# Performance work log

Hardware: AMD Instinct MI355X
Metric: run time of the kernel (lower is better)

Reference implementation:

```python
import jax, jax.numpy as jnp
import numpy as np

RADIUS = 400.0
FIELD = 8000.0  # um extent of slide coordinate field


def setup_inputs() -> dict:
    key = jax.random.key(0)
    ks = jax.random.split(key, 8)
    B, N, D, H, K = 4, 4096, 1536, 512, 8
    images = jax.random.normal(ks[0], (B, N, D), dtype=jnp.float32)
    positions = jax.random.uniform(ks[1], (B, N, 2), dtype=jnp.float32) * FIELD
    W_feat = jax.random.normal(ks[2], (D, H), dtype=jnp.float32) * (1.0 / np.sqrt(D))
    b_feat = jnp.zeros((H,), dtype=jnp.float32)
    W_pos = jax.random.normal(ks[3], (2, H), dtype=jnp.float32) * 0.5
    W_gnn = jax.random.normal(ks[4], (H, H), dtype=jnp.float32) * (1.0 / np.sqrt(H))
    W_self = jax.random.normal(ks[5], (H, H), dtype=jnp.float32) * (1.0 / np.sqrt(H))
    anchors = jax.random.normal(ks[6], (K, D), dtype=jnp.float32)
    return {"images": images, "positions": positions, "W_feat": W_feat,
            "b_feat": b_feat, "W_pos": W_pos, "W_gnn": W_gnn,
            "W_self": W_self, "anchors": anchors}


def _radius_adjacency(pos):
    # pos: (N, 2). Dense O(N^2) radius graph (mirrors torch.cdist + mask).
    sq = jnp.sum(pos * pos, axis=-1)                       # (N,)
    d2 = sq[:, None] + sq[None, :] - 2.0 * (pos @ pos.T)   # (N, N)
    mask = d2 < (RADIUS * RADIUS)
    N = pos.shape[0]
    mask = mask & ~jnp.eye(N, dtype=bool)                  # no self-loops
    return mask.astype(pos.dtype)


def reference(images, positions, W_feat, b_feat, W_pos, W_gnn, W_self, anchors):
    # --- Stream A: explicit concept quantifier (cosine sim to anchors) ---
    x_norm = images / jnp.clip(jnp.linalg.norm(images, axis=-1, keepdims=True), 1e-12)
    a_norm = anchors / jnp.clip(jnp.linalg.norm(anchors, axis=-1, keepdims=True), 1e-12)
    scores = jnp.einsum('bnd,kd->bnk', x_norm, a_norm)     # (B, N, K)
    concept_profile = scores.mean(axis=1)                  # (B, K)

    # --- Stream B: feature extraction with positional encoding ---
    feat = images @ W_feat + b_feat + positions @ W_pos    # (B, N, H)

    # --- radius graph + one mean-aggregation GNN layer, per slide ---
    def per_graph(f, p):
        A = _radius_adjacency(p)                           # (N, N)
        deg = jnp.clip(A.sum(axis=-1, keepdims=True), 1.0) # (N, 1)
        h = jax.nn.relu(f)
        agg = (A @ h) / deg                                # mean over neighbors
        return jax.nn.relu(agg @ W_gnn + f @ W_self)       # (N, H)

    refined = jax.vmap(per_graph)(feat, positions)         # (B, N, H)
    latent_spatial = refined.mean(axis=1)                  # (B, H)  per-graph mean pool

    return jnp.concatenate([latent_spatial, concept_profile], axis=1)  # (B, H+K)
```

## Files before the change

### kernel.cpp

```cpp
#include <hip/hip_runtime.h>

#define B_ 4
#define N_ 4096
#define D_ 1536
#define H_ 512
#define K_ 8
#define M_ (B_*N_)
#define R2_ 160000.0f

typedef __attribute__((ext_vector_type(8))) short bf16x8;
typedef __attribute__((ext_vector_type(4))) float f32x4;

__device__ __forceinline__ unsigned short f2bf(float f) {
  union { float f; unsigned u; } v; v.f = f;
  unsigned r = (v.u + 0x7FFFu + ((v.u >> 16) & 1u)) >> 16;
  return (unsigned short)r;
}
__device__ __forceinline__ float bf2f(unsigned short s) {
  union { unsigned u; float f; } v; v.u = ((unsigned)s) << 16; return v.f;
}

typedef const __attribute__((address_space(1))) unsigned int gas_u32;
typedef __attribute__((address_space(3))) unsigned int las_u32;
__device__ __forceinline__ void gl_lds16(const unsigned short* g, unsigned short* l) {
  __builtin_amdgcn_global_load_lds((gas_u32*)g, (las_u32*)l, 16, 0, 0);
}

__global__ void k_anorm(const float* __restrict__ anchors, float* __restrict__ anorm) {
  int k = blockIdx.x; int lane = threadIdx.x;
  float s = 0.f;
  for (int i = lane; i < D_; i += 64) { float v = anchors[k*D_ + i]; s += v*v; }
  #pragma unroll
  for (int off = 32; off; off >>= 1) s += __shfl_down(s, off);
  if (lane == 0) anorm[k] = fmaxf(sqrtf(s), 1e-12f);
}

__global__ void k_transpose(const float* __restrict__ W, unsigned short* __restrict__ WT,
                            int Krows, int outStride, int outOff) {
  __shared__ float t[64][65];
  int bx = blockIdx.x;
  int by = blockIdx.y;
  int tid = threadIdx.x;
  int tx = tid & 63, ty = tid >> 6;
  #pragma unroll
  for (int r = 0; r < 64; r += 4)
    t[ty + r][tx] = W[(size_t)(by*64 + ty + r)*H_ + bx*64 + tx];
  __syncthreads();
  #pragma unroll
  for (int r = 0; r < 64; r += 4) {
    int n = bx*64 + ty + r;
    WT[(size_t)n*outStride + outOff + by*64 + tx] = f2bf(t[tx][ty + r]);
  }
}

__global__ __launch_bounds__(256) void k_concept_cast(
    const float* __restrict__ images, const float* __restrict__ anchors,
    const float* __restrict__ anorm, unsigned short* __restrict__ imgs_bf,
    float* __restrict__ out) {
  __shared__ float sA[K_*D_];
  __shared__ float sc[4][K_];
  int tid = threadIdx.x, lane = tid & 63, w = tid >> 6;
  {
    const float4* a4 = (const float4*)anchors;
    float4* sA4 = (float4*)sA;
    #pragma unroll
    for (int i = 0; i < 12; i++) sA4[tid + 256*i] = a4[tid + 256*i];
  }
  __syncthreads();
  float acc_k[K_] = {};
  for (int r = 0; r < 8; r++) {
    int gm = blockIdx.x*32 + w*8 + r;
    const float4* xrow = (const float4*)(images + (size_t)gm*D_);
    float nrm = 0.f; float dot[K_] = {};
    #pragma unroll
    for (int it = 0; it < 6; it++) {
      int j = lane + 64*it;
      float4 x = xrow[j];
      nrm += x.x*x.x + x.y*x.y + x.z*x.z + x.w*x.w;
      #pragma unroll
      for (int k = 0; k < K_; k++) {
        float4 a = *(const float4*)&sA[(size_t)(k*384 + j)*4];
        dot[k] += x.x*a.x + x.y*a.y + x.z*a.z + x.w*a.w;
      }
      ushort4 s;
      s.x = f2bf(x.x); s.y = f2bf(x.y); s.z = f2bf(x.z); s.w = f2bf(x.w);
      *(ushort4*)&imgs_bf[(size_t)gm*D_ + (size_t)j*4] = s;
    }
    #pragma unroll
    for (int off = 32; off; off >>= 1) {
      nrm += __shfl_down(nrm, off);
      #pragma unroll
      for (int k = 0; k < K_; k++) dot[k] += __shfl_down(dot[k], off);
    }
    if (lane == 0) {
      float inv = 1.0f / fmaxf(sqrtf(nrm), 1e-12f);
      #pragma unroll
      for (int k = 0; k < K_; k++) acc_k[k] += dot[k] * inv / anorm[k];
    }
  }
  if (lane == 0) {
    #pragma unroll
    for (int k = 0; k < K_; k++) sc[w][k] = acc_k[k];
  }
  __syncthreads();
  if (tid < K_) {
    float s = sc[0][tid] + sc[1][tid] + sc[2][tid] + sc[3][tid];
    int b = blockIdx.x >> 7;
    atomicAdd(out + b*(H_+K_) + H_ + tid, s * (1.0f/N_));
  }
}

#define BM 128
#define BN 128
#define BK 32

__global__ __launch_bounds__(256) void k_gemm(
    const unsigned short* __restrict__ A, const unsigned short* __restrict__ BT,
    int Kdim, int mode, const float* __restrict__ bias, const float* __restrict__ Wpos,
    const float* __restrict__ positions, unsigned short* __restrict__ AB,
    float* __restrict__ out) {
  __shared__ unsigned short As[BM*BK];
  __shared__ unsigned short Bs[BN*BK];
  __shared__ float colsum[BN];
  int tid = threadIdx.x;
  int lane = tid & 63, wv = tid >> 6;
  int wm = wv >> 1, wn = wv & 1;
  int l15 = lane & 15, quad = lane >> 4;
  int bx = blockIdx.x;
  int bm = bx & 127, bn = bx >> 7;
  int m0 = bm*BM, n0 = bn*BN;

  f32x4 acc[4][4] = {};

  int c = wv*2;
  int rowc = (lane >> 2), seg = lane & 3;
  const unsigned short* gA0 = A  + (size_t)(m0 + c*16 + rowc)*Kdim + seg*8;
  const unsigned short* gA1 = gA0 + (size_t)16*Kdim;
  const unsigned short* gB0 = BT + (size_t)(n0 + c*16 + rowc)*Kdim + seg*8;
  const unsigned short* gB1 = gB0 + (size_t)16*Kdim;
  unsigned short* lA0 = As + c*512;
  unsigned short* lA1 = lA0 + 512;
  unsigned short* lB0 = Bs + c*512;
  unsigned short* lB1 = lB0 + 512;

  int nk = Kdim / BK;
  for (int kt = 0; kt < nk; kt++) {
    __syncthreads();
    gl_lds16(gA0, lA0); gl_lds16(gA1, lA1);
    gl_lds16(gB0, lB0); gl_lds16(gB1, lB1);
    gA0 += BK; gA1 += BK; gB0 += BK; gB1 += BK;
    __syncthreads();

    bf16x8 aF[4], bF[4];
    #pragma unroll
    for (int f = 0; f < 4; f++)
      aF[f] = *(const bf16x8*)&As[(wm*64 + f*16 + l15)*BK + quad*8];
    #pragma unroll
    for (int f = 0; f < 4; f++)
      bF[f] = *(const bf16x8*)&Bs[(wn*64 + f*16 + l15)*BK + quad*8];
    #pragma unroll
    for (int mi = 0; mi < 4; mi++)
      #pragma unroll
      for (int ni = 0; ni < 4; ni++)
        acc[mi][ni] = __builtin_amdgcn_mfma_f32_16x16x32_bf16(aF[mi], bF[ni], acc[mi][ni], 0, 0, 0);
  }

  if (mode == 0) {
    #pragma unroll
    for (int ni = 0; ni < 4; ni++) {
      int gh = n0 + wn*64 + ni*16 + l15;
      float bz = bias[gh];
      float w0 = Wpos[gh];
      float w1 = Wpos[H_ + gh];
      #pragma unroll
      for (int mi = 0; mi < 4; mi++) {
        #pragma unroll
        for (int r = 0; r < 4; r++) {
          int gm = m0 + wm*64 + mi*16 + quad*4 + r;
          float px = positions[(size_t)gm*2];
          float py = positions[(size_t)gm*2 + 1];
          float v = acc[mi][ni][r] + bz + px*w0 + py*w1;
          AB[(size_t)gm*1024 + 512 + gh] = f2bf(v);
        }
      }
    }
  } else {
    if (tid < BN) colsum[tid] = 0.f;
    __syncthreads();
    #pragma unroll
    for (int ni = 0; ni < 4; ni++) {
      float s = 0.f;
      #pragma unroll
      for (int mi = 0; mi < 4; mi++) {
        #pragma unroll
        for (int r = 0; r < 4; r++) s += fmaxf(acc[mi][ni][r], 0.f);
      }
      s += __shfl_down(s, 32);
      s += __shfl_down(s, 16);
      if (quad == 0) atomicAdd(&colsum[wn*64 + ni*16 + l15], s);
    }
    __syncthreads();
    if (tid < BN) {
      int b = m0 >> 12;
      atomicAdd(out + b*(H_+K_) + n0 + tid, colsum[tid] * (1.0f/N_));
    }
  }
}

__global__ void k_aggregate(const float* __restrict__ positions,
                            unsigned short* __restrict__ AB) {
  __shared__ unsigned short nlist[N_];
  __shared__ int cnt;
  int gm = blockIdx.x;
  int b = gm >> 12, i = gm & 4095;
  int tid = threadIdx.x;
  if (tid == 0) cnt = 0;
  __syncthreads();
  const float* pos = positions + (size_t)b*N_*2;
  float xi = pos[(size_t)i*2], yi = pos[(size_t)i*2 + 1];
  for (int j = tid; j < N_; j += 256) {
    float dx = pos[(size_t)j*2] - xi;
    float dy = pos[(size_t)j*2 + 1] - yi;
    float d2 = dx*dx + dy*dy;
    if (d2 < R2_ && j != i) {
      int p = atomicAdd(&cnt, 1);
      nlist[p] = (unsigned short)j;
    }
  }
  __syncthreads();
  int deg = cnt;
  float inv = 1.0f / (float)(deg > 1 ? deg : 1);
  float a0 = 0.f, a1 = 0.f;
  const unsigned short* featbase = AB + (size_t)(b << 12)*1024 + 512 + tid*2;
  for (int n = 0; n < deg; n++) {
    int j = nlist[n];
    unsigned v = *(const unsigned*)(featbase + (size_t)j*1024);
    a0 += fmaxf(bf2f((unsigned short)(v & 0xFFFFu)), 0.f);
    a1 += fmaxf(bf2f((unsigned short)(v >> 16)), 0.f);
  }
  unsigned o0 = f2bf(a0*inv), o1 = f2bf(a1*inv);
  *(unsigned*)(AB + (size_t)gm*1024 + tid*2) = (o1 << 16) | o0;
}

extern "C" void kernel_launch(void* const* d_in, const int* in_sizes, int n_in,
                              void* d_out, int out_size, void* d_ws, size_t ws_size,
                              hipStream_t stream) {
  const float* images    = (const float*)d_in[0];
  const float* positions = (const float*)d_in[1];
  const float* W_feat    = (const float*)d_in[2];
  const float* b_feat    = (const float*)d_in[3];
  const float* W_pos     = (const float*)d_in[4];
  const float* W_gnn     = (const float*)d_in[5];
  const float* W_self    = (const float*)d_in[6];
  const float* anchors   = (const float*)d_in[7];
  float* out = (float*)d_out;

  char* ws = (char*)d_ws;
  unsigned short* imgs_bf = (unsigned short*)ws;
  unsigned short* AB      = (unsigned short*)(ws + 50331648);
  unsigned short* WfT     = (unsigned short*)(ws + 83886080);
  unsigned short* WgsT    = (unsigned short*)(ws + 85458944);
  float*          anorm   = (float*)(ws + 86507520);

  hipMemsetAsync(d_out, 0, sizeof(float)*B_*(H_+K_), stream);
  k_anorm<<<K_, 64, 0, stream>>>(anchors, anorm);
  k_transpose<<<dim3(8, 24), 256, 0, stream>>>(W_feat, WfT, D_, D_, 0);
  k_transpose<<<dim3(8, 8), 256, 0, stream>>>(W_gnn,  WgsT, H_, 1024, 0);
  k_transpose<<<dim3(8, 8), 256, 0, stream>>>(W_self, WgsT, H_, 1024, 512);
  k_concept_cast<<<M_/32, 256, 0, stream>>>(images, anchors, anorm, imgs_bf, out);
  k_gemm<<<512, 256, 0, stream>>>(imgs_bf, WfT, D_, 0, b_feat, W_pos, positions, AB, out);
  k_aggregate<<<M_, 256, 0, stream>>>(positions, AB);
  k_gemm<<<512, 256, 0, stream>>>(AB, WgsT, 1024, 1, nullptr, nullptr, nullptr, AB, out);
}
```

Before: 338.2 us.

## Batch 16 destinations per block in radius aggregation and fuse prep kernels

The aggregation kernel now processes 16 destination nodes per block: it scans the positions once for all of them, stores up to a capped number of neighbours per node, and gathers features with 16-byte vector loads. Block indices are mapped so that each XCD handles a single graph, aiming for L2 locality. The weight transposes and anchor norms are merged into one launch, and the GEMM block order is swapped so that consecutive blocks share A rows. The neighbour cap of 192 would truncate neighbour lists if any node's degree ever exceeded it.

```diff
diff --git a/kernel.cpp b/kernel.cpp
--- a/kernel.cpp
+++ b/kernel.cpp
@@ -7,6 +7,7 @@
 #define K_ 8
 #define M_ (B_*N_)
 #define R2_ 160000.0f
+#define CAP 192
 
 typedef __attribute__((ext_vector_type(8))) short bf16x8;
 typedef __attribute__((ext_vector_type(4))) float f32x4;
@@ -16,9 +17,6 @@
   unsigned r = (v.u + 0x7FFFu + ((v.u >> 16) & 1u)) >> 16;
   return (unsigned short)r;
 }
-__device__ __forceinline__ float bf2f(unsigned short s) {
-  union { unsigned u; float f; } v; v.u = ((unsigned)s) << 16; return v.f;
-}
 
 typedef const __attribute__((address_space(1))) unsigned int gas_u32;
 typedef __attribute__((address_space(3))) unsigned int las_u32;
@@ -26,30 +24,37 @@
   __builtin_amdgcn_global_load_lds((gas_u32*)g, (las_u32*)l, 16, 0, 0);
 }
 
-__global__ void k_anorm(const float* __restrict__ anchors, float* __restrict__ anorm) {
-  int k = blockIdx.x; int lane = threadIdx.x;
-  float s = 0.f;
-  for (int i = lane; i < D_; i += 64) { float v = anchors[k*D_ + i]; s += v*v; }
-  #pragma unroll
-  for (int off = 32; off; off >>= 1) s += __shfl_down(s, off);
-  if (lane == 0) anorm[k] = fmaxf(sqrtf(s), 1e-12f);
-}
-
-__global__ void k_transpose(const float* __restrict__ W, unsigned short* __restrict__ WT,
-                            int Krows, int outStride, int outOff) {
+__global__ __launch_bounds__(256) void k_prep(
+    const float* __restrict__ Wf, const float* __restrict__ Wg, const float* __restrict__ Ws,
+    const float* __restrict__ anchors, unsigned short* __restrict__ WfT,
+    unsigned short* __restrict__ WgsT, float* __restrict__ anorm) {
   __shared__ float t[64][65];
-  int bx = blockIdx.x;
-  int by = blockIdx.y;
-  int tid = threadIdx.x;
+  __shared__ float red[4];
+  int bx = blockIdx.x, by = blockIdx.y, tid = threadIdx.x;
+  if (by == 40) {
+    int k = bx;
+    float s = 0.f;
+    for (int i = tid; i < D_; i += 256) { float v = anchors[k*D_ + i]; s += v*v; }
+    #pragma unroll
+    for (int off = 32; off; off >>= 1) s += __shfl_down(s, off);
+    if ((tid & 63) == 0) red[tid >> 6] = s;
+    __syncthreads();
+    if (tid == 0) anorm[k] = fmaxf(sqrtf(red[0]+red[1]+red[2]+red[3]), 1e-12f);
+    return;
+  }
+  const float* W; unsigned short* WT; int kt, outStride, outOff;
+  if (by < 24)      { W = Wf; WT = WfT;  kt = by;      outStride = D_;   outOff = 0; }
+  else if (by < 32) { W = Wg; WT = WgsT; kt = by - 24; outStride = 1024; outOff = 0; }
+  else              { W = Ws; WT = WgsT; kt = by - 32; outStride = 1024; outOff = 512; }
   int tx = tid & 63, ty = tid >> 6;
   #pragma unroll
   for (int r = 0; r < 64; r += 4)
-    t[ty + r][tx] = W[(size_t)(by*64 + ty + r)*H_ + bx*64 + tx];
+    t[ty + r][tx] = W[(size_t)(kt*64 + ty + r)*H_ + bx*64 + tx];
   __syncthreads();
   #pragma unroll
   for (int r = 0; r < 64; r += 4) {
     int n = bx*64 + ty + r;
-    WT[(size_t)n*outStride + outOff + by*64 + tx] = f2bf(t[tx][ty + r]);
+    WT[(size_t)n*outStride + outOff + kt*64 + tx] = f2bf(t[tx][ty + r]);
   }
 }
 
@@ -127,7 +132,7 @@
   int wm = wv >> 1, wn = wv & 1;
   int l15 = lane & 15, quad = lane >> 4;
   int bx = blockIdx.x;
-  int bm = bx & 127, bn = bx >> 7;
+  int bm = bx >> 2, bn = bx & 3;
   int m0 = bm*BM, n0 = bn*BN;
 
   f32x4 acc[4][4] = {};
@@ -207,39 +212,64 @@
   }
 }
 
-__global__ void k_aggregate(const float* __restrict__ positions,
-                            unsigned short* __restrict__ AB) {
-  __shared__ unsigned short nlist[N_];
-  __shared__ int cnt;
-  int gm = blockIdx.x;
-  int b = gm >> 12, i = gm & 4095;
-  int tid = threadIdx.x;
-  if (tid == 0) cnt = 0;
-  __syncthreads();
-  const float* pos = positions + (size_t)b*N_*2;
-  float xi = pos[(size_t)i*2], yi = pos[(size_t)i*2 + 1];
-  for (int j = tid; j < N_; j += 256) {
-    float dx = pos[(size_t)j*2] - xi;
-    float dy = pos[(size_t)j*2 + 1] - yi;
-    float d2 = dx*dx + dy*dy;
-    if (d2 < R2_ && j != i) {
-      int p = atomicAdd(&cnt, 1);
-      nlist[p] = (unsigned short)j;
-    }
-  }
-  __syncthreads();
-  int deg = cnt;
-  float inv = 1.0f / (float)(deg > 1 ? deg : 1);
-  float a0 = 0.f, a1 = 0.f;
-  const unsigned short* featbase = AB + (size_t)(b << 12)*1024 + 512 + tid*2;
-  for (int n = 0; n < deg; n++) {
-    int j = nlist[n];
-    unsigned v = *(const unsigned*)(featbase + (size_t)j*1024);
-    a0 += fmaxf(bf2f((unsigned short)(v & 0xFFFFu)), 0.f);
-    a1 += fmaxf(bf2f((unsigned short)(v >> 16)), 0.f);
-  }
-  unsigned o0 = f2bf(a0*inv), o1 = f2bf(a1*inv);
-  *(unsigned*)(AB + (size_t)gm*1024 + tid*2) = (o1 << 16) | o0;
+__global__ __launch_bounds__(256) void k_aggregate(const float* __restrict__ positions,
+                                                   unsigned short* __restrict__ AB) {
+  __shared__ unsigned short nlist[16*CAP];
+  __shared__ int cnt[16];
+  __shared__ float sdx[16], sdy[16];
+  int blk = blockIdx.x;
+  int xcd = blk & 7;
+  int b = xcd >> 1;
+  int sub = ((blk >> 3) << 1) | (xcd & 1);
+  int dest0 = sub * 16;
+  int tid = threadIdx.x, lane = tid & 63, w = tid >> 6;
+  const float2* p2 = (const float2*)(positions + (size_t)b*N_*2);
+  if (tid < 16) {
+    cnt[tid] = 0;
+    float2 pd = p2[dest0 + tid];
+    sdx[tid] = pd.x; sdy[tid] = pd.y;
+  }
+  __syncthreads();
+  for (int it = 0; it < 16; it++) {
+    int j = tid + 256*it;
+    float2 pj = p2[j];
+    #pragma unroll
+    for (int d = 0; d < 16; d++) {
+      float dx = pj.x - sdx[d], dy = pj.y - sdy[d];
+      if (dx*dx + dy*dy < R2_ && j != dest0 + d) {
+        int p = atomicAdd(&cnt[d], 1);
+        if (p < CAP) nlist[d*CAP + p] = (unsigned short)j;
+      }
+    }
+  }
+  __syncthreads();
+  const unsigned short* featb = AB + ((size_t)(b << 12))*1024 + 512 + lane*8;
+  #pragma unroll
+  for (int dd = 0; dd < 4; dd++) {
+    int d = w*4 + dd;
+    int deg = cnt[d]; if (deg > CAP) deg = CAP;
+    float inv = 1.0f / (float)(deg > 1 ? deg : 1);
+    float a0=0.f,a1=0.f,a2=0.f,a3=0.f,a4=0.f,a5=0.f,a6=0.f,a7=0.f;
+    for (int n = 0; n < deg; n++) {
+      int j = nlist[d*CAP + n];
+      uint4 v = *(const uint4*)(featb + (size_t)j*1024);
+      union { unsigned u; float f; } lo, hi;
+      lo.u = v.x << 16;          hi.u = v.x & 0xFFFF0000u;
+      a0 += fmaxf(lo.f, 0.f);    a1 += fmaxf(hi.f, 0.f);
+      lo.u = v.y << 16;          hi.u = v.y & 0xFFFF0000u;
+      a2 += fmaxf(lo.f, 0.f);    a3 += fmaxf(hi.f, 0.f);
+      lo.u = v.z << 16;          hi.u = v.z & 0xFFFF0000u;
+      a4 += fmaxf(lo.f, 0.f);    a5 += fmaxf(hi.f, 0.f);
+      lo.u = v.w << 16;          hi.u = v.w & 0xFFFF0000u;
+      a6 += fmaxf(lo.f, 0.f);    a7 += fmaxf(hi.f, 0.f);
+    }
+    uint4 o;
+    o.x = ((unsigned)f2bf(a1*inv) << 16) | f2bf(a0*inv);
+    o.y = ((unsigned)f2bf(a3*inv) << 16) | f2bf(a2*inv);
+    o.z = ((unsigned)f2bf(a5*inv) << 16) | f2bf(a4*inv);
+    o.w = ((unsigned)f2bf(a7*inv) << 16) | f2bf(a6*inv);
+    *(uint4*)(AB + (size_t)((b << 12) + dest0 + d)*1024 + lane*8) = o;
+  }
 }
 
 extern "C" void kernel_launch(void* const* d_in, const int* in_sizes, int n_in,
@@ -263,12 +293,9 @@
   float*          anorm   = (float*)(ws + 86507520);
 
   hipMemsetAsync(d_out, 0, sizeof(float)*B_*(H_+K_), stream);
-  k_anorm<<<K_, 64, 0, stream>>>(anchors, anorm);
-  k_transpose<<<dim3(8, 24), 256, 0, stream>>>(W_feat, WfT, D_, D_, 0);
-  k_transpose<<<dim3(8, 8), 256, 0, stream>>>(W_gnn,  WgsT, H_, 1024, 0);
-  k_transpose<<<dim3(8, 8), 256, 0, stream>>>(W_self, WgsT, H_, 1024, 512);
+  k_prep<<<dim3(8, 41), 256, 0, stream>>>(W_feat, W_gnn, W_self, anchors, WfT, WgsT, anorm);
   k_concept_cast<<<M_/32, 256, 0, stream>>>(images, anchors, anorm, imgs_bf, out);
   k_gemm<<<512, 256, 0, stream>>>(imgs_bf, WfT, D_, 0, b_feat, W_pos, positions, AB, out);
-  k_aggregate<<<M_, 256, 0, stream>>>(positions, AB);
+  k_aggregate<<<1024, 256, 0, stream>>>(positions, AB);
   k_gemm<<<512, 256, 0, stream>>>(AB, WgsT, 1024, 1, nullptr, nullptr, nullptr, AB, out);
 }
```

Result: faster. 318.2 us (-5.9%).
